# Optimization experiments

Measured on AMD Instinct MI355X. Metric: run time of the kernel, lower is better.

## Reference

```python
import jax, jax.numpy as jnp
import numpy as np

B, LQ, LK, D, DV = 8, 2048, 2048, 1024, 1024

def setup_inputs() -> dict:
    key0 = jax.random.key(0)
    k1, k2, k3, k4, k5 = jax.random.split(key0, 5)
    return {
        "key": jax.random.normal(k1, (B, LK, D), dtype=jnp.float32),
        "query": jax.random.normal(k2, (B, LQ, D), dtype=jnp.float32),
        "value": jax.random.normal(k3, (B, LK, DV), dtype=jnp.float32),
        "W": jax.random.normal(k4, (D, D), dtype=jnp.float32),
        "bias": jax.random.normal(k5, (1,), dtype=jnp.float32),
    }

def reference(key, query, value, W, bias):
    # bilinear scores: query @ W @ key^T  -> [B, Lq, Lk]
    qW = jnp.einsum('bqd,de->bqe', query, W)
    scores = jnp.einsum('bqe,bke->bqk', qW, key) + bias  # scalar bias broadcast
    weights = jax.nn.softmax(scores, axis=-1)
    ctx = jnp.einsum('bqk,bkv->bqv', weights, value)  # [B, Lq, Dv]
    return (weights, ctx)
```

## Files before the change

### kernel.cpp

```cpp
#include <hip/hip_runtime.h>


typedef unsigned short ushort_t;
typedef __attribute__((ext_vector_type(8))) short short8;
typedef __attribute__((ext_vector_type(4))) float f32x4;

__device__ __forceinline__ ushort_t f2bf(float f) {
    unsigned u = __float_as_uint(f);
    unsigned r = u + 0x7fff + ((u >> 16) & 1);
    return (ushort_t)(r >> 16);
}
__device__ __forceinline__ float bf2f(ushort_t h) {
    return __uint_as_float(((unsigned)h) << 16);
}

__device__ __forceinline__ void gload_lds16(const void* g, void* l) {
    __builtin_amdgcn_global_load_lds(
        (const __attribute__((address_space(1))) unsigned int*)g,
        (__attribute__((address_space(3))) unsigned int*)l,
        16, 0, 0);
}

__global__ __launch_bounds__(256) void gemm3x(
    const ushort_t* __restrict__ Ah, const ushort_t* __restrict__ Al,
    const ushort_t* __restrict__ Bh, const ushort_t* __restrict__ Bl,
    float* __restrict__ C, int K, int N, long sA, long sB, long sC)
{
    __shared__ ushort_t sAh[128 * 32], sAl[128 * 32], sBh[128 * 32], sBl[128 * 32];

    const int bz = blockIdx.z;
    Ah += (long)bz * sA; Al += (long)bz * sA;
    Bh += (long)bz * sB; Bl += (long)bz * sB;
    C  += (long)bz * sC;

    const int m0 = blockIdx.y * 128, n0 = blockIdx.x * 128;
    const int tid = threadIdx.x, w = tid >> 6, lane = tid & 63;
    const int wm = (w & 1) * 64, wn = (w >> 1) * 64;
    const int r16 = lane & 15, quad = lane >> 4;

    f32x4 acc[4][4] = {};

    const int c0 = w * 2;
    const int srow = lane >> 2;
    const int scol = (lane & 3) * 8;

    for (int k0 = 0; k0 < K; k0 += 32) {
        #pragma unroll
        for (int t = 0; t < 2; ++t) {
            const int c = c0 + t;
            const int grow = c * 16 + srow;
            const long ga = (long)(m0 + grow) * K + k0 + scol;
            const long gb = (long)(n0 + grow) * K + k0 + scol;
            gload_lds16(Ah + ga, &sAh[c * 512]);
            gload_lds16(Al + ga, &sAl[c * 512]);
            gload_lds16(Bh + gb, &sBh[c * 512]);
            gload_lds16(Bl + gb, &sBl[c * 512]);
        }
        __syncthreads();

        short8 a_h[4], a_l[4], b_h[4], b_l[4];
        #pragma unroll
        for (int i = 0; i < 4; ++i) {
            a_h[i] = *(const short8*)&sAh[(wm + i * 16 + r16) * 32 + quad * 8];
            a_l[i] = *(const short8*)&sAl[(wm + i * 16 + r16) * 32 + quad * 8];
            b_h[i] = *(const short8*)&sBh[(wn + i * 16 + r16) * 32 + quad * 8];
            b_l[i] = *(const short8*)&sBl[(wn + i * 16 + r16) * 32 + quad * 8];
        }
        #pragma unroll
        for (int i = 0; i < 4; ++i)
            #pragma unroll
            for (int j = 0; j < 4; ++j) {
                acc[i][j] = __builtin_amdgcn_mfma_f32_16x16x32_bf16(a_h[i], b_h[j], acc[i][j], 0, 0, 0);
                acc[i][j] = __builtin_amdgcn_mfma_f32_16x16x32_bf16(a_h[i], b_l[j], acc[i][j], 0, 0, 0);
                acc[i][j] = __builtin_amdgcn_mfma_f32_16x16x32_bf16(a_l[i], b_h[j], acc[i][j], 0, 0, 0);
            }
        __syncthreads();
    }

    #pragma unroll
    for (int i = 0; i < 4; ++i)
        #pragma unroll
        for (int j = 0; j < 4; ++j)
            #pragma unroll
            for (int r = 0; r < 4; ++r)
                C[(long)(m0 + wm + i * 16 + quad * 4 + r) * N + n0 + wn + j * 16 + r16] = acc[i][j][r];
}

__global__ __launch_bounds__(256) void gemm1x(
    const ushort_t* __restrict__ A, const ushort_t* __restrict__ Bt,
    float* __restrict__ C, int K, int N, long sA, long sB, long sC)
{
    __shared__ ushort_t sA_[128 * 32], sB_[128 * 32];

    const int bz = blockIdx.z;
    A += (long)bz * sA; Bt += (long)bz * sB; C += (long)bz * sC;

    const int m0 = blockIdx.y * 128, n0 = blockIdx.x * 128;
    const int tid = threadIdx.x, w = tid >> 6, lane = tid & 63;
    const int wm = (w & 1) * 64, wn = (w >> 1) * 64;
    const int r16 = lane & 15, quad = lane >> 4;

    f32x4 acc[4][4] = {};

    const int c0 = w * 2;
    const int srow = lane >> 2;
    const int scol = (lane & 3) * 8;

    for (int k0 = 0; k0 < K; k0 += 32) {
        #pragma unroll
        for (int t = 0; t < 2; ++t) {
            const int c = c0 + t;
            const int grow = c * 16 + srow;
            gload_lds16(A  + (long)(m0 + grow) * K + k0 + scol, &sA_[c * 512]);
            gload_lds16(Bt + (long)(n0 + grow) * K + k0 + scol, &sB_[c * 512]);
        }
        __syncthreads();

        short8 a_[4], b_[4];
        #pragma unroll
        for (int i = 0; i < 4; ++i) {
            a_[i] = *(const short8*)&sA_[(wm + i * 16 + r16) * 32 + quad * 8];
            b_[i] = *(const short8*)&sB_[(wn + i * 16 + r16) * 32 + quad * 8];
        }
        #pragma unroll
        for (int i = 0; i < 4; ++i)
            #pragma unroll
            for (int j = 0; j < 4; ++j)
                acc[i][j] = __builtin_amdgcn_mfma_f32_16x16x32_bf16(a_[i], b_[j], acc[i][j], 0, 0, 0);
        __syncthreads();
    }

    #pragma unroll
    for (int i = 0; i < 4; ++i)
        #pragma unroll
        for (int j = 0; j < 4; ++j)
            #pragma unroll
            for (int r = 0; r < 4; ++r)
                C[(long)(m0 + wm + i * 16 + quad * 4 + r) * N + n0 + wn + j * 16 + r16] = acc[i][j][r];
}

__global__ __launch_bounds__(256) void split_pair(
    const float* __restrict__ x, ushort_t* __restrict__ hi, ushort_t* __restrict__ lo, int n4)
{
    int i = blockIdx.x * 256 + threadIdx.x;
    if (i >= n4) return;
    float4 v = ((const float4*)x)[i];
    ushort4 h, l;
    h.x = f2bf(v.x); l.x = f2bf(v.x - bf2f(h.x));
    h.y = f2bf(v.y); l.y = f2bf(v.y - bf2f(h.y));
    h.z = f2bf(v.z); l.z = f2bf(v.z - bf2f(h.z));
    h.w = f2bf(v.w); l.w = f2bf(v.w - bf2f(h.w));
    ((ushort4*)hi)[i] = h;
    ((ushort4*)lo)[i] = l;
}

__global__ __launch_bounds__(256) void transpose_cvt(
    const float* __restrict__ src, ushort_t* __restrict__ dst,
    int R, int C, long sS, long sD)
{
    __shared__ float t[32][33];
    src += (long)blockIdx.z * sS; dst += (long)blockIdx.z * sD;
    const int r0 = blockIdx.y * 32, c0 = blockIdx.x * 32;
    const int tx = threadIdx.x & 31, ty = threadIdx.x >> 5;
    #pragma unroll
    for (int yy = 0; yy < 4; ++yy)
        t[ty + yy * 8][tx] = src[(long)(r0 + ty + yy * 8) * C + c0 + tx];
    __syncthreads();
    #pragma unroll
    for (int yy = 0; yy < 4; ++yy)
        dst[(long)(c0 + ty + yy * 8) * R + r0 + tx] = f2bf(t[tx][ty + yy * 8]);
}

__global__ __launch_bounds__(256) void transpose_split(
    const float* __restrict__ src, ushort_t* __restrict__ dstH, ushort_t* __restrict__ dstL,
    int R, int C)
{
    __shared__ float t[32][33];
    const int r0 = blockIdx.y * 32, c0 = blockIdx.x * 32;
    const int tx = threadIdx.x & 31, ty = threadIdx.x >> 5;
    #pragma unroll
    for (int yy = 0; yy < 4; ++yy)
        t[ty + yy * 8][tx] = src[(long)(r0 + ty + yy * 8) * C + c0 + tx];
    __syncthreads();
    #pragma unroll
    for (int yy = 0; yy < 4; ++yy) {
        float v = t[tx][ty + yy * 8];
        ushort_t h = f2bf(v);
        dstH[(long)(c0 + ty + yy * 8) * R + r0 + tx] = h;
        dstL[(long)(c0 + ty + yy * 8) * R + r0 + tx] = f2bf(v - bf2f(h));
    }
}

__global__ __launch_bounds__(256) void softmax_rows(
    float* __restrict__ S, ushort_t* __restrict__ Pb)
{
    __shared__ float red[256];
    const int tid = threadIdx.x;
    float4* p4 = (float4*)(S + (size_t)blockIdx.x * 2048);

    float4 x0 = p4[tid];
    float4 x1 = p4[tid + 256];

    float m = fmaxf(fmaxf(fmaxf(x0.x, x0.y), fmaxf(x0.z, x0.w)),
                    fmaxf(fmaxf(x1.x, x1.y), fmaxf(x1.z, x1.w)));
    red[tid] = m;
    __syncthreads();
    #pragma unroll
    for (int s = 128; s > 0; s >>= 1) {
        if (tid < s) red[tid] = fmaxf(red[tid], red[tid + s]);
        __syncthreads();
    }
    const float rowmax = red[0];
    __syncthreads();

    x0.x = __expf(x0.x - rowmax); x0.y = __expf(x0.y - rowmax);
    x0.z = __expf(x0.z - rowmax); x0.w = __expf(x0.w - rowmax);
    x1.x = __expf(x1.x - rowmax); x1.y = __expf(x1.y - rowmax);
    x1.z = __expf(x1.z - rowmax); x1.w = __expf(x1.w - rowmax);

    red[tid] = (x0.x + x0.y + x0.z + x0.w) + (x1.x + x1.y + x1.z + x1.w);
    __syncthreads();
    #pragma unroll
    for (int s = 128; s > 0; s >>= 1) {
        if (tid < s) red[tid] += red[tid + s];
        __syncthreads();
    }
    const float inv = 1.0f / red[0];

    x0.x *= inv; x0.y *= inv; x0.z *= inv; x0.w *= inv;
    x1.x *= inv; x1.y *= inv; x1.z *= inv; x1.w *= inv;
    p4[tid] = x0;
    p4[tid + 256] = x1;

    ushort4* pb = (ushort4*)(Pb + (size_t)blockIdx.x * 2048);
    ushort4 b0, b1;
    b0.x = f2bf(x0.x); b0.y = f2bf(x0.y); b0.z = f2bf(x0.z); b0.w = f2bf(x0.w);
    b1.x = f2bf(x1.x); b1.y = f2bf(x1.y); b1.z = f2bf(x1.z); b1.w = f2bf(x1.w);
    pb[tid] = b0;
    pb[tid + 256] = b1;
}

extern "C" void kernel_launch(void* const* d_in, const int* in_sizes, int n_in,
                              void* d_out, int out_size, void* d_ws, size_t ws_size,
                              hipStream_t stream)
{
    const float* key   = (const float*)d_in[0];
    const float* query = (const float*)d_in[1];
    const float* value = (const float*)d_in[2];
    const float* W     = (const float*)d_in[3];

    float* weights = (float*)d_out;
    float* ctx     = (float*)d_out + 33554432;

    ushort_t* Qh  = (ushort_t*)d_ws;
    ushort_t* Ql  = Qh + 16777216;
    ushort_t* Kh  = Qh + 33554432;
    ushort_t* Kl  = Qh + 50331648;
    ushort_t* Wth = Qh + 67108864;
    ushort_t* Wtl = Qh + 68157440;
    ushort_t* Pb  = Kh;
    ushort_t* Vt  = Qh;

    transpose_split<<<dim3(32, 32, 1), 256, 0, stream>>>(W, Wth, Wtl, 1024, 1024);
    split_pair<<<16384, 256, 0, stream>>>(query, Qh, Ql, 4194304);
    split_pair<<<16384, 256, 0, stream>>>(key, Kh, Kl, 4194304);
    gemm3x<<<dim3(8, 128, 1), 256, 0, stream>>>(Qh, Ql, Wth, Wtl, ctx, 1024, 1024, 0, 0, 0);
    split_pair<<<16384, 256, 0, stream>>>(ctx, Qh, Ql, 4194304);
    gemm3x<<<dim3(16, 16, 8), 256, 0, stream>>>(Qh, Ql, Kh, Kl, weights, 1024, 2048,
                                                2048L * 1024, 2048L * 1024, 2048L * 2048);
    softmax_rows<<<16384, 256, 0, stream>>>(weights, Pb);
    transpose_cvt<<<dim3(32, 64, 8), 256, 0, stream>>>(value, Vt, 2048, 1024,
                                                       2048L * 1024, 1024L * 2048);
    gemm1x<<<dim3(8, 16, 8), 256, 0, stream>>>(Pb, Vt, ctx, 2048, 1024,
                                               2048L * 2048, 2048L * 1024, 2048L * 1024);
}
```

Baseline: 863.6 us.

## Use 32x32 MFMA tiles, fuse qW split into GEMM epilogue, XCD-aware PV grid

All GEMMs switch from 16x16x32 to 32x32x16 bf16 MFMA instructions with 2x2 accumulator tiles per wave. The first GEMM now writes hi/lo bf16 halves directly in its epilogue, into the ctx output buffer as scratch, which removes the separate split_pair pass over qW. The PV GEMM uses a 1D grid remapped so that consecutive blocks sharing A strips land on the same XCD, to improve L2 reuse. The epilogue's scattered 2-byte stores and the wider accumulator layout may change store efficiency and register pressure.

```diff
diff --git a/kernel.cpp b/kernel.cpp
--- a/kernel.cpp
+++ b/kernel.cpp
@@ -3,7 +3,7 @@
 
 typedef unsigned short ushort_t;
 typedef __attribute__((ext_vector_type(8))) short short8;
-typedef __attribute__((ext_vector_type(4))) float f32x4;
+typedef __attribute__((ext_vector_type(16))) float f32x16;
 
 __device__ __forceinline__ ushort_t f2bf(float f) {
     unsigned u = __float_as_uint(f);
@@ -21,122 +21,161 @@
         16, 0, 0);
 }
 
-__global__ __launch_bounds__(256) void gemm3x(
+#define GEMM3X_BODY(EPILOGUE)                                                     \
+    __shared__ ushort_t sAh[128 * 32], sAl[128 * 32], sBh[128 * 32], sBl[128 * 32];\
+    const int bz = blockIdx.z;                                                    \
+    Ah += (long)bz * sA; Al += (long)bz * sA;                                     \
+    Bh += (long)bz * sB; Bl += (long)bz * sB;                                     \
+    const int m0 = blockIdx.y * 128, n0 = blockIdx.x * 128;                       \
+    const int tid = threadIdx.x, w = tid >> 6, lane = tid & 63;                   \
+    const int wm = (w & 1) * 64, wn = (w >> 1) * 64;                              \
+    const int l31 = lane & 31, half = lane >> 5;                                  \
+    f32x16 acc[2][2] = {};                                                        \
+    const int c0 = w * 2;                                                         \
+    const int srow = lane >> 2, scol = (lane & 3) * 8;                            \
+    for (int k0 = 0; k0 < K; k0 += 32) {                                          \
+        _Pragma("unroll")                                                         \
+        for (int t = 0; t < 2; ++t) {                                             \
+            const int c = c0 + t;                                                 \
+            const int grow = c * 16 + srow;                                       \
+            const long ga = (long)(m0 + grow) * K + k0 + scol;                    \
+            const long gb = (long)(n0 + grow) * K + k0 + scol;                    \
+            gload_lds16(Ah + ga, &sAh[c * 512]);                                  \
+            gload_lds16(Al + ga, &sAl[c * 512]);                                  \
+            gload_lds16(Bh + gb, &sBh[c * 512]);                                  \
+            gload_lds16(Bl + gb, &sBl[c * 512]);                                  \
+        }                                                                         \
+        __syncthreads();                                                          \
+        _Pragma("unroll")                                                         \
+        for (int s = 0; s < 2; ++s) {                                             \
+            short8 a_h[2], a_l[2], b_h[2], b_l[2];                                \
+            const int ko = s * 16 + half * 8;                                     \
+            _Pragma("unroll")                                                     \
+            for (int i = 0; i < 2; ++i) {                                         \
+                a_h[i] = *(const short8*)&sAh[(wm + i * 32 + l31) * 32 + ko];     \
+                a_l[i] = *(const short8*)&sAl[(wm + i * 32 + l31) * 32 + ko];     \
+                b_h[i] = *(const short8*)&sBh[(wn + i * 32 + l31) * 32 + ko];     \
+                b_l[i] = *(const short8*)&sBl[(wn + i * 32 + l31) * 32 + ko];     \
+            }                                                                     \
+            _Pragma("unroll")                                                     \
+            for (int i = 0; i < 2; ++i)                                           \
+                _Pragma("unroll")                                                 \
+                for (int j = 0; j < 2; ++j) {                                     \
+                    acc[i][j] = __builtin_amdgcn_mfma_f32_32x32x16_bf16(a_h[i], b_h[j], acc[i][j], 0, 0, 0); \
+                    acc[i][j] = __builtin_amdgcn_mfma_f32_32x32x16_bf16(a_h[i], b_l[j], acc[i][j], 0, 0, 0); \
+                    acc[i][j] = __builtin_amdgcn_mfma_f32_32x32x16_bf16(a_l[i], b_h[j], acc[i][j], 0, 0, 0); \
+                }                                                                 \
+        }                                                                         \
+        __syncthreads();                                                          \
+    }                                                                             \
+    EPILOGUE
+
+__global__ __launch_bounds__(256) void gemm3x_f32(
     const ushort_t* __restrict__ Ah, const ushort_t* __restrict__ Al,
     const ushort_t* __restrict__ Bh, const ushort_t* __restrict__ Bl,
     float* __restrict__ C, int K, int N, long sA, long sB, long sC)
 {
-    __shared__ ushort_t sAh[128 * 32], sAl[128 * 32], sBh[128 * 32], sBl[128 * 32];
-
-    const int bz = blockIdx.z;
-    Ah += (long)bz * sA; Al += (long)bz * sA;
-    Bh += (long)bz * sB; Bl += (long)bz * sB;
-    C  += (long)bz * sC;
-
-    const int m0 = blockIdx.y * 128, n0 = blockIdx.x * 128;
+    GEMM3X_BODY({
+        C += (long)bz * sC;
+        _Pragma("unroll")
+        for (int i = 0; i < 2; ++i)
+            _Pragma("unroll")
+            for (int j = 0; j < 2; ++j)
+                _Pragma("unroll")
+                for (int r = 0; r < 16; ++r) {
+                    const int row = wm + i * 32 + (r & 3) + 8 * (r >> 2) + 4 * half;
+                    const int col = wn + j * 32 + l31;
+                    C[(long)(m0 + row) * N + n0 + col] = acc[i][j][r];
+                }
+    })
+}
+
+__global__ __launch_bounds__(256) void gemm3x_split(
+    const ushort_t* __restrict__ Ah, const ushort_t* __restrict__ Al,
+    const ushort_t* __restrict__ Bh, const ushort_t* __restrict__ Bl,
+    ushort_t* __restrict__ Ch, ushort_t* __restrict__ Cl, int K, int N,
+    long sA, long sB, long sC)
+{
+    GEMM3X_BODY({
+        Ch += (long)bz * sC; Cl += (long)bz * sC;
+        _Pragma("unroll")
+        for (int i = 0; i < 2; ++i)
+            _Pragma("unroll")
+            for (int j = 0; j < 2; ++j)
+                _Pragma("unroll")
+                for (int r = 0; r < 16; ++r) {
+                    const int row = wm + i * 32 + (r & 3) + 8 * (r >> 2) + 4 * half;
+                    const int col = wn + j * 32 + l31;
+                    const long o = (long)(m0 + row) * N + n0 + col;
+                    float x = acc[i][j][r];
+                    ushort_t h = f2bf(x);
+                    Ch[o] = h;
+                    Cl[o] = f2bf(x - bf2f(h));
+                }
+    })
+}
+
+__global__ __launch_bounds__(256) void gemm1x(
+    const ushort_t* __restrict__ A, const ushort_t* __restrict__ Bt,
+    float* __restrict__ C, int K, int N, long sA, long sB, long sC, int gy)
+{
+    const int id = blockIdx.x;
+    const int xcd = id & 7, t = id >> 3;
+    const int bx = t & 7, rest = t >> 3;
+    const int strip = xcd + 8 * rest;
+    const int by = strip % gy, bz = strip / gy;
+
+    __shared__ ushort_t sA_[128 * 32], sB_[128 * 32];
+
+    A += (long)bz * sA; Bt += (long)bz * sB; C += (long)bz * sC;
+
+    const int m0 = by * 128, n0 = bx * 128;
     const int tid = threadIdx.x, w = tid >> 6, lane = tid & 63;
     const int wm = (w & 1) * 64, wn = (w >> 1) * 64;
-    const int r16 = lane & 15, quad = lane >> 4;
-
-    f32x4 acc[4][4] = {};
+    const int l31 = lane & 31, half = lane >> 5;
+
+    f32x16 acc[2][2] = {};
 
     const int c0 = w * 2;
-    const int srow = lane >> 2;
-    const int scol = (lane & 3) * 8;
+    const int srow = lane >> 2, scol = (lane & 3) * 8;
 
     for (int k0 = 0; k0 < K; k0 += 32) {
         #pragma unroll
-        for (int t = 0; t < 2; ++t) {
-            const int c = c0 + t;
-            const int grow = c * 16 + srow;
-            const long ga = (long)(m0 + grow) * K + k0 + scol;
-            const long gb = (long)(n0 + grow) * K + k0 + scol;
-            gload_lds16(Ah + ga, &sAh[c * 512]);
-            gload_lds16(Al + ga, &sAl[c * 512]);
-            gload_lds16(Bh + gb, &sBh[c * 512]);
-            gload_lds16(Bl + gb, &sBl[c * 512]);
-        }
-        __syncthreads();
-
-        short8 a_h[4], a_l[4], b_h[4], b_l[4];
-        #pragma unroll
-        for (int i = 0; i < 4; ++i) {
-            a_h[i] = *(const short8*)&sAh[(wm + i * 16 + r16) * 32 + quad * 8];
-            a_l[i] = *(const short8*)&sAl[(wm + i * 16 + r16) * 32 + quad * 8];
-            b_h[i] = *(const short8*)&sBh[(wn + i * 16 + r16) * 32 + quad * 8];
-            b_l[i] = *(const short8*)&sBl[(wn + i * 16 + r16) * 32 + quad * 8];
-        }
-        #pragma unroll
-        for (int i = 0; i < 4; ++i)
-            #pragma unroll
-            for (int j = 0; j < 4; ++j) {
-                acc[i][j] = __builtin_amdgcn_mfma_f32_16x16x32_bf16(a_h[i], b_h[j], acc[i][j], 0, 0, 0);
-                acc[i][j] = __builtin_amdgcn_mfma_f32_16x16x32_bf16(a_h[i], b_l[j], acc[i][j], 0, 0, 0);
-                acc[i][j] = __builtin_amdgcn_mfma_f32_16x16x32_bf16(a_l[i], b_h[j], acc[i][j], 0, 0, 0);
-            }
-        __syncthreads();
-    }
-
-    #pragma unroll
-    for (int i = 0; i < 4; ++i)
-        #pragma unroll
-        for (int j = 0; j < 4; ++j)
-            #pragma unroll
-            for (int r = 0; r < 4; ++r)
-                C[(long)(m0 + wm + i * 16 + quad * 4 + r) * N + n0 + wn + j * 16 + r16] = acc[i][j][r];
-}
-
-__global__ __launch_bounds__(256) void gemm1x(
-    const ushort_t* __restrict__ A, const ushort_t* __restrict__ Bt,
-    float* __restrict__ C, int K, int N, long sA, long sB, long sC)
-{
-    __shared__ ushort_t sA_[128 * 32], sB_[128 * 32];
-
-    const int bz = blockIdx.z;
-    A += (long)bz * sA; Bt += (long)bz * sB; C += (long)bz * sC;
-
-    const int m0 = blockIdx.y * 128, n0 = blockIdx.x * 128;
-    const int tid = threadIdx.x, w = tid >> 6, lane = tid & 63;
-    const int wm = (w & 1) * 64, wn = (w >> 1) * 64;
-    const int r16 = lane & 15, quad = lane >> 4;
-
-    f32x4 acc[4][4] = {};
-
-    const int c0 = w * 2;
-    const int srow = lane >> 2;
-    const int scol = (lane & 3) * 8;
-
-    for (int k0 = 0; k0 < K; k0 += 32) {
-        #pragma unroll
-        for (int t = 0; t < 2; ++t) {
-            const int c = c0 + t;
+        for (int t2 = 0; t2 < 2; ++t2) {
+            const int c = c0 + t2;
             const int grow = c * 16 + srow;
             gload_lds16(A  + (long)(m0 + grow) * K + k0 + scol, &sA_[c * 512]);
             gload_lds16(Bt + (long)(n0 + grow) * K + k0 + scol, &sB_[c * 512]);
         }
         __syncthreads();
-
-        short8 a_[4], b_[4];
         #pragma unroll
-        for (int i = 0; i < 4; ++i) {
-            a_[i] = *(const short8*)&sA_[(wm + i * 16 + r16) * 32 + quad * 8];
-            b_[i] = *(const short8*)&sB_[(wn + i * 16 + r16) * 32 + quad * 8];
+        for (int s = 0; s < 2; ++s) {
+            short8 a_[2], b_[2];
+            const int ko = s * 16 + half * 8;
+            #pragma unroll
+            for (int i = 0; i < 2; ++i) {
+                a_[i] = *(const short8*)&sA_[(wm + i * 32 + l31) * 32 + ko];
+                b_[i] = *(const short8*)&sB_[(wn + i * 32 + l31) * 32 + ko];
+            }
+            #pragma unroll
+            for (int i = 0; i < 2; ++i)
+                #pragma unroll
+                for (int j = 0; j < 2; ++j)
+                    acc[i][j] = __builtin_amdgcn_mfma_f32_32x32x16_bf16(a_[i], b_[j], acc[i][j], 0, 0, 0);
         }
-        #pragma unroll
-        for (int i = 0; i < 4; ++i)
-            #pragma unroll
-            for (int j = 0; j < 4; ++j)
-                acc[i][j] = __builtin_amdgcn_mfma_f32_16x16x32_bf16(a_[i], b_[j], acc[i][j], 0, 0, 0);
         __syncthreads();
     }
 
     #pragma unroll
-    for (int i = 0; i < 4; ++i)
+    for (int i = 0; i < 2; ++i)
         #pragma unroll
-        for (int j = 0; j < 4; ++j)
+        for (int j = 0; j < 2; ++j)
             #pragma unroll
-            for (int r = 0; r < 4; ++r)
-                C[(long)(m0 + wm + i * 16 + quad * 4 + r) * N + n0 + wn + j * 16 + r16] = acc[i][j][r];
+            for (int r = 0; r < 16; ++r) {
+                const int row = wm + i * 32 + (r & 3) + 8 * (r >> 2) + 4 * half;
+                const int col = wn + j * 32 + l31;
+                C[(long)(m0 + row) * N + n0 + col] = acc[i][j][r];
+            }
 }
 
 __global__ __launch_bounds__(256) void split_pair(
@@ -258,19 +297,22 @@
     ushort_t* Kl  = Qh + 50331648;
     ushort_t* Wth = Qh + 67108864;
     ushort_t* Wtl = Qh + 68157440;
+    ushort_t* qWh = (ushort_t*)ctx;
+    ushort_t* qWl = qWh + 16777216;
     ushort_t* Pb  = Kh;
     ushort_t* Vt  = Qh;
 
     transpose_split<<<dim3(32, 32, 1), 256, 0, stream>>>(W, Wth, Wtl, 1024, 1024);
     split_pair<<<16384, 256, 0, stream>>>(query, Qh, Ql, 4194304);
     split_pair<<<16384, 256, 0, stream>>>(key, Kh, Kl, 4194304);
-    gemm3x<<<dim3(8, 128, 1), 256, 0, stream>>>(Qh, Ql, Wth, Wtl, ctx, 1024, 1024, 0, 0, 0);
-    split_pair<<<16384, 256, 0, stream>>>(ctx, Qh, Ql, 4194304);
-    gemm3x<<<dim3(16, 16, 8), 256, 0, stream>>>(Qh, Ql, Kh, Kl, weights, 1024, 2048,
-                                                2048L * 1024, 2048L * 1024, 2048L * 2048);
+    gemm3x_split<<<dim3(8, 128, 1), 256, 0, stream>>>(Qh, Ql, Wth, Wtl, qWh, qWl,
+                                                      1024, 1024, 0, 0, 0);
+    gemm3x_f32<<<dim3(16, 16, 8), 256, 0, stream>>>(qWh, qWl, Kh, Kl, weights, 1024, 2048,
+                                                    2048L * 1024, 2048L * 1024, 2048L * 2048);
     softmax_rows<<<16384, 256, 0, stream>>>(weights, Pb);
     transpose_cvt<<<dim3(32, 64, 8), 256, 0, stream>>>(value, Vt, 2048, 1024,
                                                        2048L * 1024, 1024L * 2048);
-    gemm1x<<<dim3(8, 16, 8), 256, 0, stream>>>(Pb, Vt, ctx, 2048, 1024,
-                                               2048L * 2048, 2048L * 1024, 2048L * 1024);
-}
+    gemm1x<<<dim3(8 * 16 * 8, 1, 1), 256, 0, stream>>>(Pb, Vt, ctx, 2048, 1024,
+                                                       2048L * 2048, 2048L * 1024,
+                                                       2048L * 1024, 16);
+}
```

Measured after the change: 828.4 us. 4.1% less time.
